# Performance work log

Hardware: AMD Instinct MI355X
Metric: run time of the kernel (lower is better)

The kernel has to match this reference:

```python
import jax, jax.numpy as jnp
import numpy as np
from jax import lax

WIN = 11
SIGMA = 1.5


def _gaussian_kernel2d(win_size, channels, dtype):
    g = jnp.arange(win_size, dtype=dtype) - win_size // 2
    g = jnp.exp(-(g ** 2) / (2.0 * SIGMA ** 2))
    g = g / g.sum()
    k2 = jnp.einsum('i,j->ij', g, g)
    return jnp.broadcast_to(k2, (channels, 1, win_size, win_size))


def setup_inputs() -> dict:
    key = jax.random.key(0)
    k1, k2 = jax.random.split(key)
    B, C, H, W = 8, 19, 512, 512
    pred = jax.random.normal(k1, (B, C, H, W), dtype=jnp.float32)
    target = jax.random.randint(k2, (B, H, W), 0, C, dtype=jnp.int64)
    return {"pred": pred, "target": target}


def reference(pred, target):
    B, C, H, W = pred.shape
    win = min(H, W, WIN)
    p = jax.nn.softmax(pred, axis=1)
    t = jax.nn.one_hot(target, C, dtype=p.dtype).transpose(0, 3, 1, 2)  # [B,C,H,W]
    kernel = _gaussian_kernel2d(win, C, p.dtype)

    def dwconv(x):  # depthwise valid conv over all classes at once
        return lax.conv_general_dilated(x, kernel, (1, 1), 'VALID',
                                        feature_group_count=C)

    mu1 = dwconv(p)
    mu2 = dwconv(t)
    mu12 = mu1 * mu2
    mu1sq = mu1 * mu1
    mu2sq = mu2 * mu2
    var1 = dwconv(p * p) - mu1sq
    var2 = dwconv(t * t) - mu2sq
    covar = dwconv(p * t) - mu12

    L = 1.0
    c1 = (0.01 * L) ** 2
    c2 = (0.03 * L) ** 2
    cs = (2.0 * covar + c2) / (var1 + var2 + c2)
    ss = (2.0 * mu12 + c1) / (mu1sq + mu2sq + c1) * cs  # [B,C,H',W']

    ss = ss.reshape(B, C, -1).mean(axis=-1)  # per (batch, class) SSIM
    ss = jax.nn.relu(ss)  # nonnegative=True
    # loss = mean over classes of (1 - mean over batch of ss) == 1 - mean(ss)
    return 1.0 - ss.mean()
```

## Files before the change

### kernel.cpp

```cpp
#include <hip/hip_runtime.h>
#include <hip/hip_fp16.h>

namespace {

constexpr int B = 8, C = 19, H = 512, W = 512, HW = H * W;
constexpr int OH = 502, OW = 502;
constexpr int TH = 32, TW = 54;
constexpr int IH = 42, IW = 64;
constexpr int LW = 77;

__device__ constexpr float G[11] = {
    0.00102838f, 0.00759876f, 0.03600077f, 0.10936070f, 0.21300553f,
    0.26601173f,
    0.21300553f, 0.10936070f, 0.03600077f, 0.00759876f, 0.00102838f};


__global__ __launch_bounds__(256) void softmax_kernel(
    const float* __restrict__ pred, __half* __restrict__ pH,
    float* __restrict__ accum) {
  const int tid = blockIdx.x * 256 + threadIdx.x;
  if (blockIdx.x == 0 && threadIdx.x < B * C) accum[threadIdx.x] = 0.0f;
  const int p2 = tid * 2;
  const int b = p2 / HW;
  const int px = p2 - b * HW;
  const float* base = pred + (size_t)b * C * HW + px;
  unsigned eh[C];
  float sx = 0.f, sy = 0.f;
#pragma unroll
  for (int c = 0; c < C; ++c) {
    float2 v = *(const float2*)(base + (size_t)c * HW);
    float ex = __expf(v.x), ey = __expf(v.y);
    sx += ex;
    sy += ey;
    __half2 h = __floats2half2_rn(ex, ey);
    eh[c] = *(const unsigned*)&h;
  }
  const float rx = 1.f / sx, ry = 1.f / sy;
  __half* outb = pH + (size_t)b * C * HW + px;
#pragma unroll
  for (int c = 0; c < C; ++c) {
    __half2 h = *(const __half2*)&eh[c];
    __half2 p = __floats2half2_rn(__low2float(h) * rx, __high2float(h) * ry);
    *(unsigned*)(outb + (size_t)c * HW) = *(const unsigned*)&p;
  }
}

__global__ __launch_bounds__(256)
__attribute__((amdgpu_waves_per_eu(4, 4))) void ssim_kernel(
    const __half* __restrict__ pH, const int* __restrict__ target,
    float* __restrict__ accum) {
  __shared__ unsigned pTu[IH * IW / 2];
  __shared__ unsigned tmask[IH * IW];
  __shared__ unsigned vOutU[2][TH][LW];
  const int tid = threadIdx.x;
  const int x0 = blockIdx.x * TW;
  const int y0 = blockIdx.y * TH;
  const int z = blockIdx.z;
  const int b = z >> 2;
  const int c0 = (z & 3) * 5;
  const int c1 = min(c0 + 5, C);
  const int ow = min(TW, OW - x0);
  const int oh = min(TH, OH - y0);

  const int col = tid & 63;
  const int rg = tid >> 6;
  const int rb = rg * 8;
  const int prow = tid >> 3;
  const int cg = tid & 7;
  const int cbase = cg * 8;

  {
    const int* tb = target + b * HW;
    for (int w = tid; w < IH * IW; w += 256) {
      int r = w >> 6, cc = w & 63;
      int t = tb[min(y0 + r, H - 1) * W + min(x0 + cc, W - 1)];
      tmask[w] = 1u << t;
    }
  }
  {
    const __half* pb = pH + (size_t)(b * C + c0) * HW;
#pragma unroll
    for (int k = 0; k < 6; ++k) {
      int w = tid + k * 256;
      if (w < IH * IW / 2) {
        int r = w >> 5, cw = w & 31;
        pTu[w] = *(const unsigned*)(pb + min(y0 + r, H - 1) * W +
                                    min(x0 + 2 * cw, W - 2));
      }
    }
  }

  float* accp = accum + b * C;
  for (int c = c0; c < c1; ++c) {
    __syncthreads();

    if (rb < oh) {
      float aP[8] = {}, aP2[8] = {}, aPT[8] = {}, aT[8] = {};
#pragma unroll
      for (int j = 0; j < 18; ++j) {
        int lr = rb + j;
        float pv = __half2float(((const __half*)pTu)[lr * IW + col]);
        unsigned m = tmask[lr * IW + col];
        float tf = (float)((m >> c) & 1u);
        float p2 = pv * pv;
        float pt = tf * pv;
#pragma unroll
        for (int oo = 0; oo < 8; ++oo) {
          int g = j - oo;
          if (g >= 0 && g < 11) {
            float gw = G[g];
            aP[oo] = fmaf(gw, pv, aP[oo]);
            aP2[oo] = fmaf(gw, p2, aP2[oo]);
            aPT[oo] = fmaf(gw, pt, aPT[oo]);
            aT[oo] = fmaf(gw, tf, aT[oo]);
          }
        }
      }
#pragma unroll
      for (int oo = 0; oo < 8; ++oo) {
        int r = rb + oo;
        __half2 a = __floats2half2_rn(aP[oo], aP2[oo]);
        __half2 bb = __floats2half2_rn(aPT[oo], aT[oo]);
        vOutU[0][r][col] = *(const unsigned*)&a;
        vOutU[1][r][col] = *(const unsigned*)&bb;
      }
    }
    __syncthreads();

    const bool more = (c + 1) < c1;
    unsigned R2[6];
    if (more) {
      const __half* pn = pH + (size_t)(b * C + c + 1) * HW;
#pragma unroll
      for (int k = 0; k < 6; ++k) {
        int w = tid + k * 256;
        unsigned v = 0;
        if (w < IH * IW / 2) {
          int r = w >> 5, cw = w & 31;
          v = *(const unsigned*)(pn + min(y0 + r, H - 1) * W +
                                 min(x0 + 2 * cw, W - 2));
        }
        R2[k] = v;
      }
    }

    float acc = 0.0f;
    if (rb < oh) {
      float mu1[8] = {}, dp2[8] = {}, dpt[8] = {}, mu2[8] = {};
#pragma unroll
      for (int gsel = 0; gsel < 2; ++gsel) {
        unsigned vin[18];
#pragma unroll
        for (int k = 0; k < 18; ++k) vin[k] = vOutU[gsel][prow][cbase + k];
#pragma unroll
        for (int j = 0; j < 18; ++j) {
          __half2 hv = *(const __half2*)&vin[j];
          float lo = __low2float(hv), hi = __high2float(hv);
#pragma unroll
          for (int oo = 0; oo < 8; ++oo) {
            int g = j - oo;
            if (g >= 0 && g < 11) {
              float gw = G[g];
              if (gsel == 0) {
                mu1[oo] = fmaf(gw, lo, mu1[oo]);
                dp2[oo] = fmaf(gw, hi, dp2[oo]);
              } else {
                dpt[oo] = fmaf(gw, lo, dpt[oo]);
                mu2[oo] = fmaf(gw, hi, mu2[oo]);
              }
            }
          }
        }
      }
      if (prow < oh) {
#pragma unroll
        for (int oo = 0; oo < 8; ++oo) {
          if (cbase + oo < ow) {
            float m1 = mu1[oo], m2 = mu2[oo];
            float m1s = m1 * m1, m2s = m2 * m2, m12 = m1 * m2;
            float v1 = dp2[oo] - m1s;
            float v2 = m2 - m2s;
            float cv = dpt[oo] - m12;
            float num = (2.f * m12 + 1e-4f) * (2.f * cv + 9e-4f);
            float den = (m1s + m2s + 1e-4f) * (v1 + v2 + 9e-4f);
            acc += __fdividef(num, den);
          }
        }
      }
      for (int o2 = 32; o2 > 0; o2 >>= 1) acc += __shfl_down(acc, o2);
      if ((tid & 63) == 0) atomicAdd(accp + c, acc);
    }

    if (more) {
#pragma unroll
      for (int k = 0; k < 6; ++k) {
        int w = tid + k * 256;
        if (w < IH * IW / 2) pTu[w] = R2[k];
      }
    }
  }
}


__global__ __launch_bounds__(256) void denom_kernel(
    const float* __restrict__ pred, const int* __restrict__ target,
    float* __restrict__ rs, unsigned char* __restrict__ t8,
    float* __restrict__ accum) {
  int tid = blockIdx.x * 256 + threadIdx.x;
  if (blockIdx.x == 0 && threadIdx.x < B * C) accum[threadIdx.x] = 0.0f;
  int p4 = tid * 4;
  int b = p4 / HW;
  int px = p4 - b * HW;
  const float4* pp = (const float4*)(pred + (size_t)b * C * HW + px);
  float4 s = {0.f, 0.f, 0.f, 0.f};
#pragma unroll
  for (int c = 0; c < C; ++c) {
    float4 v = pp[c * (HW / 4)];
    s.x += __expf(v.x);
    s.y += __expf(v.y);
    s.z += __expf(v.z);
    s.w += __expf(v.w);
  }
  float4 r;
  r.x = 1.0f / s.x; r.y = 1.0f / s.y; r.z = 1.0f / s.z; r.w = 1.0f / s.w;
  ((float4*)rs)[tid] = r;
  int4 t = ((const int4*)target)[tid];
  uchar4 tc;
  tc.x = (unsigned char)t.x; tc.y = (unsigned char)t.y;
  tc.z = (unsigned char)t.z; tc.w = (unsigned char)t.w;
  ((uchar4*)t8)[tid] = tc;
}

__global__ __launch_bounds__(256)
__attribute__((amdgpu_waves_per_eu(4, 4))) void ssim_f32_kernel(
    const float* __restrict__ pred, const float* __restrict__ rs,
    const unsigned char* __restrict__ t8, float* __restrict__ accum) {
  __shared__ float vOut[4][TH][68];
  const int tid = threadIdx.x;
  const int x0 = blockIdx.x * TW;
  const int y0 = blockIdx.y * TH;
  const int z = blockIdx.z;
  const int b = z >> 2;
  const int c0 = (z & 3) * 5;
  const int c1 = min(c0 + 5, C);
  const int ow = min(TW, OW - x0);
  const int oh = min(TH, OH - y0);
  const int col = tid & 63;
  const int rg = tid >> 6;
  const int gc = min(x0 + col, W - 1);
  const int rbase = y0 + rg * 8;
  const int prow = tid >> 3;
  const int cg = tid & 7;
  const int cbase = cg * 7;
  const float* rsb = rs + b * HW;
  const unsigned char* tb = t8 + b * HW;

  for (int c = c0; c < c1; ++c) {
    __syncthreads();
    const float* pc = pred + (size_t)(b * C + c) * HW;
    float aP[8] = {}, aP2[8] = {}, aPT[8] = {}, aT[8] = {};
#pragma unroll
    for (int j = 0; j < 18; ++j) {
      int r = min(rbase + j, H - 1);
      int o = r * W + gc;
      float p = __expf(pc[o]) * rsb[o];
      float p2 = p * p;
      bool hit = ((int)tb[o] == c);
      float tf = hit ? 1.0f : 0.0f;
      float pt = hit ? p : 0.0f;
#pragma unroll
      for (int oo = 0; oo < 8; ++oo) {
        int g = j - oo;
        if (g >= 0 && g < 11) {
          float gw = G[g];
          aP[oo] = fmaf(gw, p, aP[oo]);
          aP2[oo] = fmaf(gw, p2, aP2[oo]);
          aPT[oo] = fmaf(gw, pt, aPT[oo]);
          aT[oo] = fmaf(gw, tf, aT[oo]);
        }
      }
    }
#pragma unroll
    for (int oo = 0; oo < 8; ++oo) {
      int r = rg * 8 + oo;
      vOut[0][r][col] = aP[oo];
      vOut[1][r][col] = aP2[oo];
      vOut[2][r][col] = aPT[oo];
      vOut[3][r][col] = aT[oo];
    }
    __syncthreads();

    float mres[4][7];
#pragma unroll
    for (int f = 0; f < 4; ++f) {
      float vin[17];
#pragma unroll
      for (int k = 0; k < 17; ++k) vin[k] = vOut[f][prow][cbase + k];
#pragma unroll
      for (int oo = 0; oo < 7; ++oo) {
        float s = 0.0f;
#pragma unroll
        for (int j = 0; j < 11; ++j) s = fmaf(G[j], vin[oo + j], s);
        mres[f][oo] = s;
      }
    }
    float acc = 0.0f;
    if (prow < oh) {
#pragma unroll
      for (int oo = 0; oo < 7; ++oo) {
        if (cbase + oo < ow) {
          float m1 = mres[0][oo], m2 = mres[3][oo];
          float m1s = m1 * m1, m2s = m2 * m2, m12 = m1 * m2;
          float v1 = mres[1][oo] - m1s;
          float v2 = m2 - m2s;
          float cv = mres[2][oo] - m12;
          float num = (2.f * m12 + 1e-4f) * (2.f * cv + 9e-4f);
          float den = (m1s + m2s + 1e-4f) * (v1 + v2 + 9e-4f);
          acc += __fdividef(num, den);
        }
      }
    }
    for (int o2 = 32; o2 > 0; o2 >>= 1) acc += __shfl_down(acc, o2);
    if ((tid & 63) == 0) atomicAdd(&accum[b * C + c], acc);
  }
}

__global__ __launch_bounds__(256) void finish_kernel(
    const float* __restrict__ accum, float* __restrict__ out) {
  __shared__ float red[4];
  int tid = threadIdx.x;
  float v = 0.0f;
  if (tid < B * C) {
    float m = accum[tid] * (1.0f / (float)(OH * OW));
    v = m > 0.0f ? m : 0.0f;
  }
  for (int off = 32; off > 0; off >>= 1) v += __shfl_down(v, off);
  if ((tid & 63) == 0) red[tid >> 6] = v;
  __syncthreads();
  if (tid == 0)
    out[0] = 1.0f - (red[0] + red[1] + red[2] + red[3]) / (float)(B * C);
}

}

extern "C" void kernel_launch(void* const* d_in, const int* in_sizes, int n_in,
                              void* d_out, int out_size, void* d_ws,
                              size_t ws_size, hipStream_t stream) {
  const float* pred = (const float*)d_in[0];
  const int* target = (const int*)d_in[1];
  float* out = (float*)d_out;

  const size_t needH = (size_t)B * C * HW * 2 + (size_t)B * C * 4;
  dim3 grid((OW + TW - 1) / TW, (OH + TH - 1) / TH, B * 4);

  if (ws_size >= needH) {
    __half* pH = (__half*)d_ws;
    float* accum = (float*)((char*)d_ws + (size_t)B * C * HW * 2);
    softmax_kernel<<<B * HW / 512, 256, 0, stream>>>(pred, pH, accum);
    ssim_kernel<<<grid, 256, 0, stream>>>(pH, target, accum);
    finish_kernel<<<1, 256, 0, stream>>>(accum, out);
  } else {
    float* rs = (float*)d_ws;
    unsigned char* t8 = (unsigned char*)d_ws + (size_t)B * HW * 4;
    float* accum = (float*)((char*)d_ws + (size_t)B * HW * 5);
    denom_kernel<<<B * HW / 1024, 256, 0, stream>>>(pred, target, rs, t8,
                                                    accum);
    ssim_f32_kernel<<<grid, 256, 0, stream>>>(pred, rs, t8, accum);
    finish_kernel<<<1, 256, 0, stream>>>(accum, out);
  }
}
```

Before: 692.7 us.

## Use 512-thread SSIM blocks with 4 outputs per thread and byte-packed class mask

The half-precision SSIM kernel now launches 512 threads per block, so each thread computes 4 output rows/columns instead of 8 in both the vertical and horizontal Gaussian passes. The per-pixel 32-bit one-hot class mask in shared memory becomes byte-packed class IDs, four per word, loaded with int4 vector reads, which cuts LDS use and global load instructions. The idea is more parallelism and less register pressure per thread. The cost is more redundant halo work, since each thread recomputes 14 taps for 4 outputs instead of 18 for 8. The waves_per_eu occupancy hint is also dropped.

Result: slower. 1.158 ms (+67.2%).

```diff
diff --git a/kernel.cpp b/kernel.cpp
--- a/kernel.cpp
+++ b/kernel.cpp
@@ -45,12 +45,11 @@
   }
 }
 
-__global__ __launch_bounds__(256)
-__attribute__((amdgpu_waves_per_eu(4, 4))) void ssim_kernel(
+__global__ __launch_bounds__(512) void ssim_kernel(
     const __half* __restrict__ pH, const int* __restrict__ target,
     float* __restrict__ accum) {
   __shared__ unsigned pTu[IH * IW / 2];
-  __shared__ unsigned tmask[IH * IW];
+  __shared__ unsigned tm4[IH * IW / 4];
   __shared__ unsigned vOutU[2][TH][LW];
   const int tid = threadIdx.x;
   const int x0 = blockIdx.x * TW;
@@ -64,24 +63,36 @@
 
   const int col = tid & 63;
   const int rg = tid >> 6;
-  const int rb = rg * 8;
-  const int prow = tid >> 3;
-  const int cg = tid & 7;
-  const int cbase = cg * 8;
+  const int rb = rg * 4;
+  const int prow = tid >> 4;
+  const int cg = tid & 15;
+  const int cbase = cg * 4;
 
   {
     const int* tb = target + b * HW;
-    for (int w = tid; w < IH * IW; w += 256) {
-      int r = w >> 6, cc = w & 63;
-      int t = tb[min(y0 + r, H - 1) * W + min(x0 + cc, W - 1)];
-      tmask[w] = 1u << t;
+    for (int w = tid; w < IH * IW / 4; w += 512) {
+      int p4 = w * 4;
+      int r = p4 >> 6, cc = p4 & 63;
+      int gr = min(y0 + r, H - 1) * W;
+      unsigned m;
+      if (x0 + cc + 3 <= W - 1) {
+        int4 t4 = *(const int4*)(tb + gr + x0 + cc);
+        m = (unsigned)(t4.x & 0xff) | ((unsigned)(t4.y & 0xff) << 8) |
+            ((unsigned)(t4.z & 0xff) << 16) | ((unsigned)(t4.w & 0xff) << 24);
+      } else {
+        m = 0;
+#pragma unroll
+        for (int i = 0; i < 4; ++i)
+          m |= ((unsigned)tb[gr + min(x0 + cc + i, W - 1)] & 0xffu) << (8 * i);
+      }
+      tm4[w] = m;
     }
   }
   {
     const __half* pb = pH + (size_t)(b * C + c0) * HW;
 #pragma unroll
-    for (int k = 0; k < 6; ++k) {
-      int w = tid + k * 256;
+    for (int k = 0; k < 3; ++k) {
+      int w = tid + k * 512;
       if (w < IH * IW / 2) {
         int r = w >> 5, cw = w & 31;
         pTu[w] = *(const unsigned*)(pb + min(y0 + r, H - 1) * W +
@@ -95,17 +106,18 @@
     __syncthreads();
 
     if (rb < oh) {
-      float aP[8] = {}, aP2[8] = {}, aPT[8] = {}, aT[8] = {};
-#pragma unroll
-      for (int j = 0; j < 18; ++j) {
+      float aP[4] = {}, aP2[4] = {}, aPT[4] = {}, aT[4] = {};
+#pragma unroll
+      for (int j = 0; j < 14; ++j) {
         int lr = rb + j;
         float pv = __half2float(((const __half*)pTu)[lr * IW + col]);
-        unsigned m = tmask[lr * IW + col];
-        float tf = (float)((m >> c) & 1u);
+        unsigned m = tm4[(lr * IW + col) >> 2];
+        unsigned cls = (m >> ((col & 3) * 8)) & 0xffu;
+        float tf = (cls == (unsigned)c) ? 1.0f : 0.0f;
         float p2 = pv * pv;
         float pt = tf * pv;
 #pragma unroll
-        for (int oo = 0; oo < 8; ++oo) {
+        for (int oo = 0; oo < 4; ++oo) {
           int g = j - oo;
           if (g >= 0 && g < 11) {
             float gw = G[g];
@@ -117,7 +129,7 @@
         }
       }
 #pragma unroll
-      for (int oo = 0; oo < 8; ++oo) {
+      for (int oo = 0; oo < 4; ++oo) {
         int r = rb + oo;
         __half2 a = __floats2half2_rn(aP[oo], aP2[oo]);
         __half2 bb = __floats2half2_rn(aPT[oo], aT[oo]);
@@ -128,12 +140,12 @@
     __syncthreads();
 
     const bool more = (c + 1) < c1;
-    unsigned R2[6];
+    unsigned R2[3];
     if (more) {
       const __half* pn = pH + (size_t)(b * C + c + 1) * HW;
 #pragma unroll
-      for (int k = 0; k < 6; ++k) {
-        int w = tid + k * 256;
+      for (int k = 0; k < 3; ++k) {
+        int w = tid + k * 512;
         unsigned v = 0;
         if (w < IH * IW / 2) {
           int r = w >> 5, cw = w & 31;
@@ -145,19 +157,19 @@
     }
 
     float acc = 0.0f;
-    if (rb < oh) {
-      float mu1[8] = {}, dp2[8] = {}, dpt[8] = {}, mu2[8] = {};
+    {
+      float mu1[4] = {}, dp2[4] = {}, dpt[4] = {}, mu2[4] = {};
 #pragma unroll
       for (int gsel = 0; gsel < 2; ++gsel) {
-        unsigned vin[18];
-#pragma unroll
-        for (int k = 0; k < 18; ++k) vin[k] = vOutU[gsel][prow][cbase + k];
-#pragma unroll
-        for (int j = 0; j < 18; ++j) {
+        unsigned vin[14];
+#pragma unroll
+        for (int k = 0; k < 14; ++k) vin[k] = vOutU[gsel][prow][cbase + k];
+#pragma unroll
+        for (int j = 0; j < 14; ++j) {
           __half2 hv = *(const __half2*)&vin[j];
           float lo = __low2float(hv), hi = __high2float(hv);
 #pragma unroll
-          for (int oo = 0; oo < 8; ++oo) {
+          for (int oo = 0; oo < 4; ++oo) {
             int g = j - oo;
             if (g >= 0 && g < 11) {
               float gw = G[g];
@@ -174,7 +186,7 @@
       }
       if (prow < oh) {
 #pragma unroll
-        for (int oo = 0; oo < 8; ++oo) {
+        for (int oo = 0; oo < 4; ++oo) {
           if (cbase + oo < ow) {
             float m1 = mu1[oo], m2 = mu2[oo];
             float m1s = m1 * m1, m2s = m2 * m2, m12 = m1 * m2;
@@ -187,14 +199,14 @@
           }
         }
       }
-      for (int o2 = 32; o2 > 0; o2 >>= 1) acc += __shfl_down(acc, o2);
-      if ((tid & 63) == 0) atomicAdd(accp + c, acc);
-    }
+    }
+    for (int o2 = 32; o2 > 0; o2 >>= 1) acc += __shfl_down(acc, o2);
+    if ((tid & 63) == 0) atomicAdd(accp + c, acc);
 
     if (more) {
 #pragma unroll
-      for (int k = 0; k < 6; ++k) {
-        int w = tid + k * 256;
+      for (int k = 0; k < 3; ++k) {
+        int w = tid + k * 512;
         if (w < IH * IW / 2) pTu[w] = R2[k];
       }
     }
@@ -231,8 +243,7 @@
   ((uchar4*)t8)[tid] = tc;
 }
 
-__global__ __launch_bounds__(256)
-__attribute__((amdgpu_waves_per_eu(4, 4))) void ssim_f32_kernel(
+__global__ __launch_bounds__(256) void ssim_f32_kernel(
     const float* __restrict__ pred, const float* __restrict__ rs,
     const unsigned char* __restrict__ t8, float* __restrict__ accum) {
   __shared__ float vOut[4][TH][68];
@@ -357,7 +368,7 @@
     __half* pH = (__half*)d_ws;
     float* accum = (float*)((char*)d_ws + (size_t)B * C * HW * 2);
     softmax_kernel<<<B * HW / 512, 256, 0, stream>>>(pred, pH, accum);
-    ssim_kernel<<<grid, 256, 0, stream>>>(pH, target, accum);
+    ssim_kernel<<<grid, 512, 0, stream>>>(pH, target, accum);
     finish_kernel<<<1, 256, 0, stream>>>(accum, out);
   } else {
     float* rs = (float*)d_ws;
```
